# Kernel tuning notes

Measured on AMD Instinct MI355X. Metric: run time of the kernel, lower is better.

The kernel has to match this reference:

```python
import jax, jax.numpy as jnp
import numpy as np

B, H, W, C = 32, 56, 56, 384
WS, SS, NH = 7, 3, 12
HD = C // NH
SCALE = HD ** -0.5
N = WS * WS
NW = (H // WS) * (W // WS)
HIDDEN = 4 * C
EPS = 1e-5


def _rel_pos_index():
    coords = np.stack(np.meshgrid(np.arange(WS), np.arange(WS), indexing='ij')).reshape(2, -1)
    rel = coords[:, :, None] - coords[:, None, :]
    rel = rel.transpose(1, 2, 0).astype(np.int64)
    rel[..., 0] += WS - 1
    rel[..., 1] += WS - 1
    rel[..., 0] *= 2 * WS - 1
    return rel.sum(-1)  # [N, N]


def _attn_mask():
    img = np.zeros((H, W), dtype=np.float32)
    slices = (slice(0, -WS), slice(-WS, -SS), slice(-SS, None))
    cnt = 0
    for hs in slices:
        for ws_ in slices:
            img[hs, ws_] = cnt
            cnt += 1
    mw = img.reshape(H // WS, WS, W // WS, WS).transpose(0, 2, 1, 3).reshape(-1, N)  # [nW, N]
    am = mw[:, None, :] - mw[:, :, None]
    return np.where(am != 0, -100.0, 0.0).astype(np.float32)  # [nW, N, N]


REL_IDX = jnp.asarray(_rel_pos_index())
ATTN_MASK = jnp.asarray(_attn_mask())


def _ln(x, g, b):
    mu = x.mean(-1, keepdims=True)
    var = ((x - mu) ** 2).mean(-1, keepdims=True)
    return (x - mu) * jax.lax.rsqrt(var + EPS) * g + b


def setup_inputs() -> dict:
    key = jax.random.key(0)
    ks = jax.random.split(key, 16)
    s = 0.02
    return {
        'x': jax.random.normal(ks[0], (B, H * W, C), jnp.float32),
        'norm1_g': jnp.ones((C,), jnp.float32),
        'norm1_b': jnp.zeros((C,), jnp.float32),
        'qkv_w': jax.random.normal(ks[1], (C, 3 * C), jnp.float32) * s,
        'qkv_b': jnp.zeros((3 * C,), jnp.float32),
        'bias_table': jax.random.normal(ks[2], ((2 * WS - 1) ** 2, NH), jnp.float32) * s,
        'proj_w': jax.random.normal(ks[3], (C, C), jnp.float32) * s,
        'proj_b': jnp.zeros((C,), jnp.float32),
        'norm2_g': jnp.ones((C,), jnp.float32),
        'norm2_b': jnp.zeros((C,), jnp.float32),
        'fc1_w': jax.random.normal(ks[4], (C, HIDDEN), jnp.float32) * s,
        'fc1_b': jnp.zeros((HIDDEN,), jnp.float32),
        'fc2_w': jax.random.normal(ks[5], (HIDDEN, C), jnp.float32) * s,
        'fc2_b': jnp.zeros((C,), jnp.float32),
    }


def reference(x, norm1_g, norm1_b, qkv_w, qkv_b, bias_table, proj_w, proj_b,
              norm2_g, norm2_b, fc1_w, fc1_b, fc2_w, fc2_b):
    shortcut = x
    h = _ln(x, norm1_g, norm1_b).reshape(B, H, W, C)
    # cyclic shift
    h = jnp.roll(h, shift=(-SS, -SS), axis=(1, 2))
    # window partition -> [B*nW, N, C]
    hw = h.reshape(B, H // WS, WS, W // WS, WS, C).transpose(0, 1, 3, 2, 4, 5).reshape(-1, N, C)
    Bw = hw.shape[0]
    # qkv
    qkv = (hw @ qkv_w + qkv_b).reshape(Bw, N, 3, NH, HD).transpose(2, 0, 3, 1, 4)
    q, k, v = qkv[0] * SCALE, qkv[1], qkv[2]  # [Bw, NH, N, HD]
    attn = jnp.einsum('whnd,whmd->whnm', q, k)
    rel_bias = bias_table[REL_IDX.reshape(-1)].reshape(N, N, NH).transpose(2, 0, 1)
    attn = attn + rel_bias[None]
    # shift mask: [Bw] = [B, nW]
    attn = attn.reshape(B, NW, NH, N, N) + ATTN_MASK[None, :, None]
    attn = jax.nn.softmax(attn.reshape(Bw, NH, N, N), axis=-1)
    o = jnp.einsum('whnm,whmd->whnd', attn, v).transpose(0, 2, 1, 3).reshape(Bw, N, C)
    o = o @ proj_w + proj_b
    # window reverse + reverse shift
    o = o.reshape(B, H // WS, W // WS, WS, WS, C).transpose(0, 1, 3, 2, 4, 5).reshape(B, H, W, C)
    o = jnp.roll(o, shift=(SS, SS), axis=(1, 2)).reshape(B, H * W, C)
    x = shortcut + o
    # MLP
    m = _ln(x, norm2_g, norm2_b)
    m = jax.nn.gelu(m @ fc1_w + fc1_b, approximate=False)
    m = m @ fc2_w + fc2_b
    return x + m
```

## Files before the change

kernel.cpp:

```cpp
#include <hip/hip_runtime.h>
#include <hip/hip_bf16.h>
#include <cstdint>
#include <cstddef>

static constexpr int Bv  = 32;
static constexpr int Cv  = 384;
static constexpr int Nv  = 49;
static constexpr int Mv  = 32 * 64 * 49;
static constexpr float SCALEv = 0.17677669529663687f;

using bf16 = __hip_bfloat16;
typedef __bf16 bf16x8 __attribute__((ext_vector_type(8)));
typedef float  f32x4  __attribute__((ext_vector_type(4)));

__global__ __launch_bounds__(256)
void wt_kernel(const float* __restrict__ w, bf16* __restrict__ wt, int K, int N) {
    int idx = blockIdx.x * 256 + threadIdx.x;
    if (idx >= K * N) return;
    int n = idx / K, k = idx - n * K;
    wt[idx] = (bf16)w[(size_t)k * N + n];
}

__global__ __launch_bounds__(256)
void bm_kernel(const float* __restrict__ btab, float* __restrict__ bmt) {
    const int cls = blockIdx.x, h = blockIdx.y;
    for (int idx = threadIdx.x; idx < 4096; idx += 256) {
        int col = idx >> 6, row = idx & 63;
        float v;
        if (col >= 49) {
            v = -1e30f;
        } else {
            int n = row < 49 ? row : 48;
            int m = col;
            int i1 = n / 7, j1 = n - i1 * 7;
            int i2 = m / 7, j2 = m - i2 * 7;
            v = btab[((i1 - i2 + 6) * 13 + (j1 - j2 + 6)) * 12 + h];
            int lh1 = (cls & 2) ? (i1 < 4 ? 1 : 2) : 0;
            int lw1 = (cls & 1) ? (j1 < 4 ? 1 : 2) : 0;
            int lh2 = (cls & 2) ? (i2 < 4 ? 1 : 2) : 0;
            int lw2 = (cls & 1) ? (j2 < 4 ? 1 : 2) : 0;
            if ((lh1 * 3 + lw1) != (lh2 * 3 + lw2)) v += -100.f;
        }
        bmt[((size_t)(cls * 12 + h) * 64 + col) * 64 + row] = v;
    }
}

template <int MODE>
__global__ __launch_bounds__(256)
void ln_kernel(const float* __restrict__ src, const float* __restrict__ gam,
               const float* __restrict__ bet, bf16* __restrict__ dst) {
    const int wave = threadIdx.x >> 6, lane = threadIdx.x & 63;
    const int r = blockIdx.x * 4 + wave;
    size_t srow;
    if (MODE == 0) {
        int w  = r / 49, n = r - w * 49;
        int b  = w >> 6, win = w & 63;
        int hb = win >> 3, wb = win & 7;
        int ii = n / 7, jj = n - ii * 7;
        int hh = hb * 7 + ii + 3; if (hh >= 56) hh -= 56;
        int ww = wb * 7 + jj + 3; if (ww >= 56) ww -= 56;
        srow = (size_t)b * 3136 + hh * 56 + ww;
    } else {
        srow = (size_t)r;
    }
    const float* p = src + srow * 384;
    float vals[6];
    float s = 0.f, s2 = 0.f;
#pragma unroll
    for (int t = 0; t < 6; ++t) {
        float v = p[t * 64 + lane];
        vals[t] = v; s += v; s2 += v * v;
    }
#pragma unroll
    for (int o = 32; o > 0; o >>= 1) {
        s  += __shfl_xor(s,  o, 64);
        s2 += __shfl_xor(s2, o, 64);
    }
    const float mu  = s * (1.f / 384.f);
    const float var = s2 * (1.f / 384.f) - mu * mu;
    const float rs  = rsqrtf(var + 1e-5f);
    bf16* q = dst + (size_t)r * 384;
#pragma unroll
    for (int t = 0; t < 6; ++t) {
        int e = t * 64 + lane;
        q[e] = (bf16)((vals[t] - mu) * rs * gam[e] + bet[e]);
    }
}

__global__ __launch_bounds__(64)
void attn_kernel(const bf16* __restrict__ qkv, const float* __restrict__ bmt,
                 bf16* __restrict__ o) {
    const int w = blockIdx.x;
    const int h = blockIdx.y;
    const int lane = threadIdx.x;
    const int quad = lane >> 4, l16 = lane & 15;
    __shared__ bf16 Vt[32][72];
    __shared__ bf16 Ps[64][72];

    const size_t rowbase = (size_t)w * 49;

    for (int idx = lane; idx < 49 * 16; idx += 64) {
        int row = idx >> 4, dp = (idx & 15) << 1;
        const bf16* src = qkv + (rowbase + row) * 1152 + 768 + h * 32 + dp;
        Vt[dp][row]     = src[0];
        Vt[dp + 1][row] = src[1];
    }
    for (int idx = lane; idx < 512; idx += 64) {
        int d = idx >> 4, c = idx & 15;
        if (c) Vt[d][48 + c] = (bf16)0.f;
    }

    f32x4 acc[4][4] = {};
    bf16x8 af[4], bfr[4];
#pragma unroll
    for (int i = 0; i < 4; ++i) {
        int row = 16 * i + l16; if (row > 48) row = 48;
        af[i] = *(const bf16x8*)(qkv + (rowbase + row) * 1152 + h * 32 + quad * 8);
    }
#pragma unroll
    for (int j = 0; j < 4; ++j) {
        int row = 16 * j + l16; if (row > 48) row = 48;
        bfr[j] = *(const bf16x8*)(qkv + (rowbase + row) * 1152 + 384 + h * 32 + quad * 8);
    }
#pragma unroll
    for (int i = 0; i < 4; ++i)
#pragma unroll
        for (int j = 0; j < 4; ++j)
            acc[i][j] = __builtin_amdgcn_mfma_f32_16x16x32_bf16(af[i], bfr[j], acc[i][j], 0, 0, 0);

    const int cls = (((w & 63) >= 56) ? 2 : 0) + (((w & 7) == 7) ? 1 : 0);
    const float* bmbase = bmt + (size_t)(cls * 12 + h) * 4096;
    float inv[4][4];
#pragma unroll
    for (int i = 0; i < 4; ++i) {
        f32x4 bm[4];
#pragma unroll
        for (int j = 0; j < 4; ++j)
            bm[j] = *(const f32x4*)(bmbase + (16 * j + l16) * 64 + 16 * i + quad * 4);
#pragma unroll
        for (int t = 0; t < 4; ++t) {
            float v0 = acc[i][0][t] + bm[0][t];
            float v1 = acc[i][1][t] + bm[1][t];
            float v2 = acc[i][2][t] + bm[2][t];
            float v3 = acc[i][3][t] + bm[3][t];
            float mx = fmaxf(fmaxf(v0, v1), fmaxf(v2, v3));
#pragma unroll
            for (int ofs = 1; ofs < 16; ofs <<= 1) mx = fmaxf(mx, __shfl_xor(mx, ofs, 64));
            float p0 = __expf(v0 - mx), p1 = __expf(v1 - mx);
            float p2 = __expf(v2 - mx), p3 = __expf(v3 - mx);
            float s = (p0 + p1) + (p2 + p3);
#pragma unroll
            for (int ofs = 1; ofs < 16; ofs <<= 1) s += __shfl_xor(s, ofs, 64);
            inv[i][t] = 1.f / s;
            int prow = 16 * i + quad * 4 + t;
            Ps[prow][l16]      = (bf16)p0;
            Ps[prow][16 + l16] = (bf16)p1;
            Ps[prow][32 + l16] = (bf16)p2;
            Ps[prow][48 + l16] = (bf16)p3;
        }
    }
    __syncthreads();

    f32x4 oacc[4][2] = {};
    bf16x8 vb[2][2];
#pragma unroll
    for (int jn = 0; jn < 2; ++jn)
#pragma unroll
        for (int ks = 0; ks < 2; ++ks)
            vb[jn][ks] = *(const bf16x8*)(&Vt[16 * jn + l16][32 * ks + quad * 8]);
#pragma unroll
    for (int i = 0; i < 4; ++i) {
#pragma unroll
        for (int ks = 0; ks < 2; ++ks) {
            bf16x8 pa = *(const bf16x8*)(&Ps[16 * i + l16][32 * ks + quad * 8]);
#pragma unroll
            for (int jn = 0; jn < 2; ++jn)
                oacc[i][jn] = __builtin_amdgcn_mfma_f32_16x16x32_bf16(pa, vb[jn][ks], oacc[i][jn], 0, 0, 0);
        }
    }

#pragma unroll
    for (int i = 0; i < 4; ++i) {
        int nbase = 16 * i + quad * 4;
#pragma unroll
        for (int t = 0; t < 4; ++t) {
            int n = nbase + t;
            if (n < 49) {
                bf16* dst = o + (rowbase + n) * 384 + h * 32;
                dst[l16]      = (bf16)(oacc[i][0][t] * inv[i][t]);
                dst[16 + l16] = (bf16)(oacc[i][1][t] * inv[i][t]);
            }
        }
    }
}

template <int EPI>
__global__ __launch_bounds__(256)
void gemm_bt(const bf16* __restrict__ A, const bf16* __restrict__ Bt,
             const float* __restrict__ bias, int N, int K,
             bf16* __restrict__ outb, float* __restrict__ outf,
             const float* __restrict__ resid) {
    __shared__ bf16 As[2][128 * 64];
    __shared__ bf16 Bs[2][128 * 64];
    const int tid  = threadIdx.x;
    const int lane = tid & 63, wave = tid >> 6;
    const int quad = lane >> 4, l16 = lane & 15;
    const int wm = wave >> 1, wn = wave & 1;

    const int nbx = gridDim.x;
    const int nwg = nbx * (int)gridDim.y;
    const int ord = (int)blockIdx.y * nbx + (int)blockIdx.x;
    const int cpx = nwg >> 3;
    const int work = (ord & 7) * cpx + (ord >> 3);
    const int by = work / nbx;
    const int bx = work - by * nbx;
    const long m0 = (long)by * 128;
    const long n0 = (long)bx * 128;

    f32x4 acc[4][4] = {};
    const int nk = K >> 6;

    auto stage = [&](int buf, int k0) {
#pragma unroll
        for (int it = 0; it < 4; ++it) {
            int e = it * 256 + tid;
            int row = e >> 3;
            int col = (e & 7) << 3;
            __builtin_amdgcn_global_load_lds(
                (const __attribute__((address_space(1))) unsigned int*)(A + (size_t)(m0 + row) * K + k0 + col),
                (__attribute__((address_space(3))) unsigned int*)(&As[buf][(size_t)e * 8]),
                16, 0, 0);
            __builtin_amdgcn_global_load_lds(
                (const __attribute__((address_space(1))) unsigned int*)(Bt + (size_t)(n0 + row) * K + k0 + col),
                (__attribute__((address_space(3))) unsigned int*)(&Bs[buf][(size_t)e * 8]),
                16, 0, 0);
        }
    };

    stage(0, 0);
    __syncthreads();

    int cur = 0;
    for (int kt = 0; kt < nk; ++kt) {
        if (kt + 1 < nk) stage(cur ^ 1, (kt + 1) * 64);
        const bf16* Ap = As[cur];
        const bf16* Bp = Bs[cur];
#pragma unroll
        for (int kk = 0; kk < 64; kk += 32) {
            bf16x8 af[4], bfr[4];
#pragma unroll
            for (int i = 0; i < 4; ++i)
                af[i] = *(const bf16x8*)(Ap + (wm * 64 + i * 16 + l16) * 64 + kk + quad * 8);
#pragma unroll
            for (int j = 0; j < 4; ++j)
                bfr[j] = *(const bf16x8*)(Bp + (wn * 64 + j * 16 + l16) * 64 + kk + quad * 8);
#pragma unroll
            for (int i = 0; i < 4; ++i)
#pragma unroll
                for (int j = 0; j < 4; ++j)
                    acc[i][j] = __builtin_amdgcn_mfma_f32_16x16x32_bf16(af[i], bfr[j], acc[i][j], 0, 0, 0);
        }
        __syncthreads();
        cur ^= 1;
    }

#pragma unroll
    for (int i = 0; i < 4; ++i) {
        const long mbase = m0 + wm * 64 + i * 16 + quad * 4;
#pragma unroll
        for (int j = 0; j < 4; ++j) {
            const int col = (int)n0 + wn * 64 + j * 16 + l16;
            const float bv = bias[col];
            f32x4 r = acc[i][j];
#pragma unroll
            for (int t = 0; t < 4; ++t) {
                const long m = mbase + t;
                float val = r[t] + bv;
                if constexpr (EPI == 0) {
                    float sc = (col < 384) ? SCALEv : 1.0f;
                    outb[(size_t)m * N + col] = (bf16)(val * sc);
                } else if constexpr (EPI == 1) {
                    int w  = (int)(m / 49), n = (int)(m - (long)w * 49);
                    int b  = w >> 6, win = w & 63;
                    int hb = win >> 3, wb = win & 7;
                    int ii = n / 7, jj = n - ii * 7;
                    int hh = hb * 7 + ii + 3; if (hh >= 56) hh -= 56;
                    int ww = wb * 7 + jj + 3; if (ww >= 56) ww -= 56;
                    size_t dst = ((size_t)b * 3136 + hh * 56 + ww) * 384 + col;
                    outf[dst] = resid[dst] + val;
                } else if constexpr (EPI == 2) {
                    float g = 0.5f * val * (1.0f + erff(val * 0.70710678118654752f));
                    outb[(size_t)m * N + col] = (bf16)g;
                } else {
                    size_t oo = (size_t)m * N + col;
                    outf[oo] = resid[oo] + val;
                }
            }
        }
    }
}

extern "C" void kernel_launch(void* const* d_in, const int* in_sizes, int n_in,
                              void* d_out, int out_size, void* d_ws, size_t ws_size,
                              hipStream_t stream) {
    const float* x     = (const float*)d_in[0];
    const float* n1g   = (const float*)d_in[1];
    const float* n1b   = (const float*)d_in[2];
    const float* qkvw  = (const float*)d_in[3];
    const float* qkvb  = (const float*)d_in[4];
    const float* btab  = (const float*)d_in[5];
    const float* projw = (const float*)d_in[6];
    const float* projb = (const float*)d_in[7];
    const float* n2g   = (const float*)d_in[8];
    const float* n2b   = (const float*)d_in[9];
    const float* fc1w  = (const float*)d_in[10];
    const float* fc1b  = (const float*)d_in[11];
    const float* fc2w  = (const float*)d_in[12];
    const float* fc2b  = (const float*)d_in[13];
    float* out = (float*)d_out;

    char* ws = (char*)d_ws;
    size_t off = 0;
    auto take = [&](size_t bytes) {
        char* p = ws + off;
        off += (bytes + 255) & ~(size_t)255;
        return p;
    };
    bf16* qkv_wt  = (bf16*)take((size_t)1152 * 384 * 2);
    bf16* proj_wt = (bf16*)take((size_t)384 * 384 * 2);
    bf16* fc1_wt  = (bf16*)take((size_t)1536 * 384 * 2);
    bf16* fc2_wt  = (bf16*)take((size_t)384 * 1536 * 2);
    float* bmt    = (float*)take((size_t)4 * 12 * 64 * 64 * 4);
    bf16* qkv_buf = (bf16*)take((size_t)Mv * 1152 * 2);
    bf16* o_buf   = (bf16*)take((size_t)Mv * 384 * 2);
    bf16* hw_buf  = (bf16*)take((size_t)Mv * 384 * 2);
    float* x1     = (float*)take((size_t)Mv * 384 * 4);
    bf16* g_buf   = qkv_buf;
    bf16* x1n     = hw_buf;

    wt_kernel<<<(384 * 1152 + 255) / 256, 256, 0, stream>>>(qkvw,  qkv_wt,  384, 1152);
    wt_kernel<<<(384 * 384  + 255) / 256, 256, 0, stream>>>(projw, proj_wt, 384, 384);
    wt_kernel<<<(384 * 1536 + 255) / 256, 256, 0, stream>>>(fc1w,  fc1_wt,  384, 1536);
    wt_kernel<<<(1536 * 384 + 255) / 256, 256, 0, stream>>>(fc2w,  fc2_wt,  1536, 384);
    bm_kernel<<<dim3(4, 12), 256, 0, stream>>>(btab, bmt);
    ln_kernel<0><<<Mv / 4, 256, 0, stream>>>(x, n1g, n1b, hw_buf);
    gemm_bt<0><<<dim3(1152 / 128, Mv / 128), 256, 0, stream>>>(
        hw_buf, qkv_wt, qkvb, 1152, 384, qkv_buf, nullptr, nullptr);
    attn_kernel<<<dim3(2048, 12), 64, 0, stream>>>(qkv_buf, bmt, o_buf);
    gemm_bt<1><<<dim3(384 / 128, Mv / 128), 256, 0, stream>>>(
        o_buf, proj_wt, projb, 384, 384, nullptr, x1, x);
    ln_kernel<1><<<Mv / 4, 256, 0, stream>>>(x1, n2g, n2b, x1n);
    gemm_bt<2><<<dim3(1536 / 128, Mv / 128), 256, 0, stream>>>(
        x1n, fc1_wt, fc1b, 1536, 384, g_buf, nullptr, nullptr);
    gemm_bt<3><<<dim3(384 / 128, Mv / 128), 256, 0, stream>>>(
        g_buf, fc2_wt, fc2b, 384, 1536, nullptr, out, x1);
}
```

Baseline: 1.319 ms.

## Load GEMM MFMA fragments directly from global memory, dropping LDS staging

Removes the double-buffered LDS staging in the bf16 GEMM kernel. Each wave now reads its A and B fragments straight from global memory into registers, with no barriers between k-tiles. This cuts LDS traffic and synchronisation. In exchange, data reuse across waves now depends on the L1/L2 caches, and global loads are no longer overlapped with compute through explicit prefetch.

```diff
diff --git a/kernel.cpp b/kernel.cpp
--- a/kernel.cpp
+++ b/kernel.cpp
@@ -200,8 +200,6 @@
              const float* __restrict__ bias, int N, int K,
              bf16* __restrict__ outb, float* __restrict__ outf,
              const float* __restrict__ resid) {
-    __shared__ bf16 As[2][128 * 64];
-    __shared__ bf16 Bs[2][128 * 64];
     const int tid  = threadIdx.x;
     const int lane = tid & 63, wave = tid >> 6;
     const int quad = lane >> 4, l16 = lane & 15;
@@ -218,50 +216,32 @@
     const long n0 = (long)bx * 128;
 
     f32x4 acc[4][4] = {};
-    const int nk = K >> 6;
-
-    auto stage = [&](int buf, int k0) {
-#pragma unroll
-        for (int it = 0; it < 4; ++it) {
-            int e = it * 256 + tid;
-            int row = e >> 3;
-            int col = (e & 7) << 3;
-            __builtin_amdgcn_global_load_lds(
-                (const __attribute__((address_space(1))) unsigned int*)(A + (size_t)(m0 + row) * K + k0 + col),
-                (__attribute__((address_space(3))) unsigned int*)(&As[buf][(size_t)e * 8]),
-                16, 0, 0);
-            __builtin_amdgcn_global_load_lds(
-                (const __attribute__((address_space(1))) unsigned int*)(Bt + (size_t)(n0 + row) * K + k0 + col),
-                (__attribute__((address_space(3))) unsigned int*)(&Bs[buf][(size_t)e * 8]),
-                16, 0, 0);
-        }
-    };
-
-    stage(0, 0);
-    __syncthreads();
-
-    int cur = 0;
-    for (int kt = 0; kt < nk; ++kt) {
-        if (kt + 1 < nk) stage(cur ^ 1, (kt + 1) * 64);
-        const bf16* Ap = As[cur];
-        const bf16* Bp = Bs[cur];
+
+    const bf16* ap[4];
+    const bf16* bp[4];
+#pragma unroll
+    for (int i = 0; i < 4; ++i)
+        ap[i] = A + (size_t)(m0 + wm * 64 + i * 16 + l16) * K + quad * 8;
+#pragma unroll
+    for (int j = 0; j < 4; ++j)
+        bp[j] = Bt + (size_t)(n0 + wn * 64 + j * 16 + l16) * K + quad * 8;
+
+    for (int k0 = 0; k0 < K; k0 += 64) {
 #pragma unroll
         for (int kk = 0; kk < 64; kk += 32) {
             bf16x8 af[4], bfr[4];
 #pragma unroll
             for (int i = 0; i < 4; ++i)
-                af[i] = *(const bf16x8*)(Ap + (wm * 64 + i * 16 + l16) * 64 + kk + quad * 8);
+                af[i] = *(const bf16x8*)(ap[i] + k0 + kk);
 #pragma unroll
             for (int j = 0; j < 4; ++j)
-                bfr[j] = *(const bf16x8*)(Bp + (wn * 64 + j * 16 + l16) * 64 + kk + quad * 8);
+                bfr[j] = *(const bf16x8*)(bp[j] + k0 + kk);
 #pragma unroll
             for (int i = 0; i < 4; ++i)
 #pragma unroll
                 for (int j = 0; j < 4; ++j)
                     acc[i][j] = __builtin_amdgcn_mfma_f32_16x16x32_bf16(af[i], bfr[j], acc[i][j], 0, 0, 0);
         }
-        __syncthreads();
-        cur ^= 1;
     }
 
 #pragma unroll
```

Measured after the change: 1.859 ms. 40.9% more time.
